# Performance work log

Hardware: AMD Instinct MI355X
Metric: run time of the kernel (lower is better)

The kernel has to match this reference:

```python
import jax, jax.numpy as jnp
import numpy as np

IN, H, F2, OUT, B = 257, 400, 600, 257, 16384


def setup_inputs() -> dict:
    key = jax.random.key(0)
    ks = jax.random.split(key, 32)
    n = lambda i, shape, s: jax.random.normal(ks[i], shape, jnp.float32) * s
    d = {
        "x": n(0, (IN, B), 1.0),
        "h1": n(1, (H, B), 1.0),
        "h2": n(2, (H, B), 1.0),
        # fc1: 257 -> 400
        "W_fc1": n(3, (H, IN), 0.05),
        "b_fc1": n(4, (H,), 0.05),
        # GRU layer 1 (hidden 400)
        "Wiz1": n(5, (H, H), 0.05), "Wir1": n(6, (H, H), 0.05), "Win1": n(7, (H, H), 0.05),
        "Whz1": n(8, (H, H), 0.05), "Whr1": n(9, (H, H), 0.05), "Whn1": n(10, (H, H), 0.05),
        "biz1": n(11, (H,), 0.05), "bir1": n(12, (H,), 0.05), "bin1": n(13, (H,), 0.05),
        "bhz1": n(14, (H,), 0.05), "bhr1": n(15, (H,), 0.05), "bhn1": n(16, (H,), 0.05),
        # GRU layer 2
        "Wiz2": n(17, (H, H), 0.05), "Wir2": n(18, (H, H), 0.05), "Win2": n(19, (H, H), 0.05),
        "Whz2": n(20, (H, H), 0.05), "Whr2": n(21, (H, H), 0.05), "Whn2": n(22, (H, H), 0.05),
        "biz2": n(23, (H,), 0.05), "bir2": n(24, (H,), 0.05), "bin2": n(25, (H,), 0.05),
        "bhz2": n(26, (H,), 0.05), "bhr2": n(27, (H,), 0.05), "bhn2": n(28, (H,), 0.05),
        # fc2: 400 -> 600, fc3: 600 -> 600, fc4: 600 -> 257
        "W_fc2": n(29, (F2, H), 0.05), "b_fc2": n(30, (F2,), 0.05),
        "W_fc3": n(31, (F2, F2), 0.05), "b_fc3": jnp.zeros((F2,), jnp.float32),
        "W_fc4": jax.random.normal(jax.random.fold_in(key, 100), (OUT, F2), jnp.float32) * 0.05,
        "b_fc4": jnp.zeros((OUT,), jnp.float32),
    }
    return d


def _gru_cell(xin, h, Wiz, Wir, Win, Whz, Whr, Whn, biz, bir, bin_, bhz, bhr, bhn):
    # xin: [H, B], h: [H, B]; column-vector convention W @ x, matching the source.
    r = jax.nn.sigmoid(Wir @ xin + bir[:, None] + Whr @ h + bhr[:, None])
    z = jax.nn.sigmoid(Wiz @ xin + biz[:, None] + Whz @ h + bhz[:, None])
    n_ = jnp.tanh(Win @ xin + bin_[:, None] + r * (Whn @ h + bhn[:, None]))
    return (1.0 - z) * n_ + z * h


def reference(x, h1, h2, W_fc1, b_fc1,
              Wiz1, Wir1, Win1, Whz1, Whr1, Whn1,
              biz1, bir1, bin1, bhz1, bhr1, bhn1,
              Wiz2, Wir2, Win2, Whz2, Whr2, Whn2,
              biz2, bir2, bin2, bhz2, bhr2, bhn2,
              W_fc2, b_fc2, W_fc3, b_fc3, W_fc4, b_fc4):
    fc1 = W_fc1 @ x + b_fc1[:, None]                       # [400, B]
    h1n = _gru_cell(fc1, h1, Wiz1, Wir1, Win1, Whz1, Whr1, Whn1,
                    biz1, bir1, bin1, bhz1, bhr1, bhn1)    # [400, B]
    h2n = _gru_cell(h1n, h2, Wiz2, Wir2, Win2, Whz2, Whr2, Whn2,
                    biz2, bir2, bin2, bhz2, bhr2, bhn2)    # [400, B]
    y = jax.nn.relu(W_fc2 @ h2n + b_fc2[:, None])          # [600, B]
    y = jax.nn.relu(W_fc3 @ y + b_fc3[:, None])            # [600, B]
    return jax.nn.sigmoid(W_fc4 @ y + b_fc4[:, None])      # [257, B]
```

## Files before the change

### kernel.cpp

```cpp
#include <hip/hip_runtime.h>
#include <math.h>


#define B_TOTAL 16384
#define H16_TOTAL 3452928L
#define PREP_TOTAL 3460352L

typedef _Float16 h8 __attribute__((ext_vector_type(8)));
typedef _Float16 h4 __attribute__((ext_vector_type(4)));
typedef float f4 __attribute__((ext_vector_type(4)));

#define GLL(g, l) __builtin_amdgcn_global_load_lds(                         \
    (const __attribute__((address_space(1))) void*)(g),                     \
    (__attribute__((address_space(3))) void*)(l), 16, 0, 0)

__device__ inline int swzg(int row, int c) { return row * 8 + (c ^ (row & 7)); }

__device__ inline void swz_bt_mt(int bid, int& bt, int& mt) {
  const int xcd = bid & 7;
  const int i = bid >> 3;
  bt = xcd * 16 + (i & 15);
  mt = i >> 4;
}

__constant__ int kJsrc[32] = {3, 5,6,7, 8,9,10, 17,18,19, 20,21,22, 29, 31, 33,
                              4, 11,12,13, 14,15,16, 23,24,25, 26,27,28, 30, 32, 34};
__constant__ int kJM[32]   = {400, 400,400,400, 400,400,400, 400,400,400, 400,400,400, 600, 600, 257,
                              400, 400,400,400, 400,400,400, 400,400,400, 400,400,400, 600, 600, 257};
__constant__ int kJK[32]   = {257, 400,400,400, 400,400,400, 400,400,400, 400,400,400, 400, 600, 600,
                              1,1,1,1, 1,1,1, 1,1,1, 1,1,1, 1, 1, 1};
__constant__ int kJKp[32]  = {320, 448,448,448, 448,448,448, 448,448,448, 448,448,448, 448, 640, 640,
                              1,1,1,1, 1,1,1, 1,1,1, 1,1,1, 1, 1, 1};
__constant__ long kJcum[33] = {0,143360,344064,544768,745472,946176,1146880,1347584,1548288,1748992,
  1949696,2150400,2351104,2551808,2838528,3248128,3452928,3453376,3453824,3454272,3454720,3455168,
  3455616,3456064,3456512,3456960,3457408,3457856,3458304,3458752,3459392,3460032,3460352};

struct SrcPtrs { const float* p[35]; };

__global__ __launch_bounds__(256) void prep_weights(SrcPtrs sp, _Float16* __restrict__ w16,
                                                    float* __restrict__ b32) {
  long w = (long)blockIdx.x * 256 + threadIdx.x;
  if (w >= PREP_TOTAL) return;
  int j = 0;
  #pragma unroll 1
  while (j < 31 && kJcum[j + 1] <= w) j++;
  long local = w - kJcum[j];
  int Kp = kJKp[j];
  int m = (int)(local / Kp);
  int k = (int)(local - (long)m * Kp);
  float v = 0.f;
  if (m < kJM[j] && k < kJK[j]) v = sp.p[kJsrc[j]][(long)m * kJK[j] + k];
  if (j < 16) w16[w] = (_Float16)v;
  else        b32[w - H16_TOTAL] = v;
}

__global__ __launch_bounds__(256) void transpose_in(const float* __restrict__ x,
                                                    const float* __restrict__ h1,
                                                    const float* __restrict__ h2,
                                                    _Float16* __restrict__ dx,
                                                    _Float16* __restrict__ dh1,
                                                    _Float16* __restrict__ dh2) {
  __shared__ float t[32][33];
  int b = blockIdx.x;
  const float* src; _Float16* dst; int F, nFT;
  if (b < 5120)        { src = x;  dst = dx;  F = 257; nFT = 10; }
  else if (b < 12288)  { b -= 5120;  src = h1; dst = dh1; F = 400; nFT = 14; }
  else                 { b -= 12288; src = h2; dst = dh2; F = 400; nFT = 14; }
  const int Fp = nFT * 32;
  const int ft = b % nFT;
  const int bt = b / nFT;
  const int ci = threadIdx.x & 31, ri = threadIdx.x >> 5;
  #pragma unroll
  for (int p = 0; p < 4; ++p) {
    int f = ft * 32 + ri + p * 8;
    float v = (f < F) ? src[(long)f * B_TOTAL + bt * 32 + ci] : 0.f;
    t[ri + p * 8][ci] = v;
  }
  __syncthreads();
  #pragma unroll
  for (int p = 0; p < 4; ++p) {
    int bb = bt * 32 + ri + p * 8;
    dst[(long)bb * Fp + ft * 32 + ci] = (_Float16)t[ci][ri + p * 8];
  }
}

__global__ __launch_bounds__(256) void transpose_out(const float* __restrict__ src,
                                                     float* __restrict__ dst) {
  __shared__ float t[32][33];
  const int nFT = 10;
  const int ft = blockIdx.x % nFT;
  const int bt = blockIdx.x / nFT;
  const int ci = threadIdx.x & 31, ri = threadIdx.x >> 5;
  #pragma unroll
  for (int p = 0; p < 4; ++p)
    t[ri + p * 8][ci] = src[(long)(bt * 32 + ri + p * 8) * 320 + ft * 32 + ci];
  __syncthreads();
  #pragma unroll
  for (int p = 0; p < 4; ++p) {
    int f = ft * 32 + ri + p * 8;
    if (f < 257) dst[(long)f * B_TOTAL + bt * 32 + ci] = t[ci][ri + p * 8];
  }
}

template <int ACT, int OUTF32>
__global__ __launch_bounds__(256) void gemm_tn(const _Float16* __restrict__ A,
                                               const _Float16* __restrict__ W,
                                               const float* __restrict__ bias,
                                               void* __restrict__ C, int K, int M) {
  __shared__ __align__(16) _Float16 As2[2][128 * 64];
  __shared__ __align__(16) _Float16 Ws2[2][64 * 64];
  const int tid = threadIdx.x;
  const int l = tid & 63;
  const int w = tid >> 6;
  int bt, mt;
  swz_bt_mt(blockIdx.x, bt, mt);
  const int wr = w >> 1, wc = w & 1;
  const int sc = ((l & 7) ^ (l >> 3)) * 8;

  const _Float16* ag = A + (long)(bt * 128 + w * 32 + (l >> 3)) * K + sc;
  const _Float16* wg = W + (long)(mt * 64 + w * 16 + (l >> 3)) * K + sc;

  f4 acc[4][2];
  #pragma unroll
  for (int i = 0; i < 4; ++i)
    #pragma unroll
    for (int jj = 0; jj < 2; ++jj) acc[i][jj] = (f4){0.f, 0.f, 0.f, 0.f};

  const int lg = l >> 4;
  const int arow = wr * 64 + (l & 15);
  const int wrow = wc * 32 + (l & 15);
  const int KT = K >> 6;

  auto stage = [&](int b, int kt) {
    const _Float16* s = ag + kt * 64;
    char* ab = (char*)(As2[b]) + w * 4096;
    #pragma unroll
    for (int i = 0; i < 4; ++i) GLL(s + (long)i * 8 * K, ab + i * 1024);
    const _Float16* s2 = wg + kt * 64;
    char* wb = (char*)(Ws2[b]) + w * 2048;
    #pragma unroll
    for (int i = 0; i < 2; ++i) GLL(s2 + (long)i * 8 * K, wb + i * 1024);
  };

  stage(0, 0);
  __syncthreads();
  int cur = 0;
  for (int t = 0; t < KT; ++t) {
    if (t + 1 < KT) stage(cur ^ 1, t + 1);
    const h8* AsV = (const h8*)(As2[cur]);
    const h8* WsV = (const h8*)(Ws2[cur]);
    h8 bfr[2][2];
    #pragma unroll
    for (int fn = 0; fn < 2; ++fn) {
      bfr[fn][0] = WsV[swzg(wrow + fn * 16, lg)];
      bfr[fn][1] = WsV[swzg(wrow + fn * 16, 4 | lg)];
    }
    #pragma unroll
    for (int fm = 0; fm < 4; ++fm) {
      h8 a0 = AsV[swzg(arow + fm * 16, lg)];
      h8 a1 = AsV[swzg(arow + fm * 16, 4 | lg)];
      #pragma unroll
      for (int fn = 0; fn < 2; ++fn) {
        acc[fm][fn] = __builtin_amdgcn_mfma_f32_16x16x32_f16(a0, bfr[fn][0], acc[fm][fn], 0, 0, 0);
        acc[fm][fn] = __builtin_amdgcn_mfma_f32_16x16x32_f16(a1, bfr[fn][1], acc[fm][fn], 0, 0, 0);
      }
    }
    __syncthreads();
    cur ^= 1;
  }

  const int colBase = mt * 64 + wc * 32 + (l & 15);
  const int rowBase = bt * 128 + wr * 64 + (l >> 4) * 4;
  #pragma unroll
  for (int fn = 0; fn < 2; ++fn) {
    const float bb = bias[colBase + fn * 16];
    #pragma unroll
    for (int fm = 0; fm < 4; ++fm) {
      #pragma unroll
      for (int r = 0; r < 4; ++r) {
        float x = acc[fm][fn][r] + bb;
        if (ACT == 1) x = fmaxf(x, 0.f);
        if (ACT == 2) x = 1.f / (1.f + __expf(-x));
        const long off = (long)(rowBase + fm * 16 + r) * M + colBase + fn * 16;
        if (OUTF32) ((float*)C)[off] = x;
        else        ((_Float16*)C)[off] = (_Float16)x;
      }
    }
  }
}

__global__ __launch_bounds__(256) void gemm_gru(const _Float16* __restrict__ Ax,
                                                const _Float16* __restrict__ Ah,
                                                const _Float16* __restrict__ Wi_,
                                                const _Float16* __restrict__ Wh_,
                                                const float* __restrict__ bi,
                                                const float* __restrict__ bh,
                                                _Float16* __restrict__ Hn) {
  __shared__ __align__(16) _Float16 As2[2][128 * 64];
  __shared__ __align__(16) _Float16 Ws2[2][3][64 * 64];
  const int tid = threadIdx.x;
  const int l = tid & 63;
  const int w = tid >> 6;
  int bt, mt;
  swz_bt_mt(blockIdx.x, bt, mt);
  const int wr = w >> 1, wc = w & 1;
  const int sc = ((l & 7) ^ (l >> 3)) * 8;

  const long arowg = (long)(bt * 128 + w * 32 + (l >> 3)) * 448 + sc;
  const long wrowg = (long)(mt * 64 + w * 16 + (l >> 3)) * 448 + sc;

  f4 acc[3][4][2];
  #pragma unroll
  for (int g = 0; g < 3; ++g)
    #pragma unroll
    for (int i = 0; i < 4; ++i)
      #pragma unroll
      for (int jj = 0; jj < 2; ++jj) acc[g][i][jj] = (f4){0.f, 0.f, 0.f, 0.f};
  h4 nxp[4][2];

  const int lg = l >> 4;
  const int arow = wr * 64 + (l & 15);
  const int wrow = wc * 32 + (l & 15);
  const int colBase = mt * 64 + wc * 32 + (l & 15);
  const float bnx0 = bi[896 + colBase], bnx1 = bi[896 + colBase + 16];

  auto stage = [&](int b, int kt) {
    const int kh = kt >= 7;
    const _Float16* As_ = kh ? Ah : Ax;
    const _Float16* Ws_ = kh ? Wh_ : Wi_;
    const int kc = (kt - (kh ? 7 : 0)) * 64;
    const _Float16* s = As_ + arowg + kc;
    char* ab = (char*)(As2[b]) + w * 4096;
    #pragma unroll
    for (int i = 0; i < 4; ++i) GLL(s + (long)i * 8 * 448, ab + i * 1024);
    const _Float16* s2 = Ws_ + wrowg + kc;
    char* wb = (char*)(Ws2[b]) + w * 2048;
    #pragma unroll
    for (int g = 0; g < 3; ++g) {
      GLL(s2 + (long)g * 200704, wb + g * 8192);
      GLL(s2 + (long)g * 200704 + 8 * 448, wb + g * 8192 + 1024);
    }
  };

  auto ktOf = [&](int i) { return i < 7 ? i : 7 + ((mt + i - 6) % 7); };

  stage(0, 0);
  __syncthreads();
  int cur = 0;
  for (int i = 0; i < 14; ++i) {
    if (i < 13) stage(cur ^ 1, ktOf(i + 1));
    const h8* AsV = (const h8*)(As2[cur]);
    const h8* WsV = (const h8*)(Ws2[cur][0]);
    h8 a[4][2];
    #pragma unroll
    for (int fm = 0; fm < 4; ++fm) {
      a[fm][0] = AsV[swzg(arow + fm * 16, lg)];
      a[fm][1] = AsV[swzg(arow + fm * 16, 4 | lg)];
    }
    #pragma unroll
    for (int g = 0; g < 3; ++g) {
      h8 b00 = WsV[g * 512 + swzg(wrow, lg)];
      h8 b01 = WsV[g * 512 + swzg(wrow, 4 | lg)];
      h8 b10 = WsV[g * 512 + swzg(wrow + 16, lg)];
      h8 b11 = WsV[g * 512 + swzg(wrow + 16, 4 | lg)];
      #pragma unroll
      for (int fm = 0; fm < 4; ++fm) {
        acc[g][fm][0] = __builtin_amdgcn_mfma_f32_16x16x32_f16(a[fm][0], b00, acc[g][fm][0], 0, 0, 0);
        acc[g][fm][0] = __builtin_amdgcn_mfma_f32_16x16x32_f16(a[fm][1], b01, acc[g][fm][0], 0, 0, 0);
        acc[g][fm][1] = __builtin_amdgcn_mfma_f32_16x16x32_f16(a[fm][0], b10, acc[g][fm][1], 0, 0, 0);
        acc[g][fm][1] = __builtin_amdgcn_mfma_f32_16x16x32_f16(a[fm][1], b11, acc[g][fm][1], 0, 0, 0);
      }
    }
    if (i == 6) {
      #pragma unroll
      for (int fm = 0; fm < 4; ++fm)
        #pragma unroll
        for (int fn = 0; fn < 2; ++fn) {
          const float bb = fn ? bnx1 : bnx0;
          #pragma unroll
          for (int r = 0; r < 4; ++r) nxp[fm][fn][r] = (_Float16)(acc[2][fm][fn][r] + bb);
          acc[2][fm][fn] = (f4){0.f, 0.f, 0.f, 0.f};
        }
    }
    __syncthreads();
    if (i < 13) cur ^= 1;
  }

  const _Float16* Alast = As2[cur];
  const int jloc = wc * 32 + (l & 15);
  const int rowLoc = wr * 64 + (l >> 4) * 4;
  const long rowGlob = (long)bt * 128 + rowLoc;
  #pragma unroll
  for (int fn = 0; fn < 2; ++fn) {
    const int j = colBase + fn * 16;
    const float bz = bi[j] + bh[j];
    const float br = bi[448 + j] + bh[448 + j];
    const float bnh = bh[896 + j];
    #pragma unroll
    for (int fm = 0; fm < 4; ++fm) {
      #pragma unroll
      for (int r = 0; r < 4; ++r) {
        const float zz = 1.f / (1.f + __expf(-(acc[0][fm][fn][r] + bz)));
        const float rr = 1.f / (1.f + __expf(-(acc[1][fm][fn][r] + br)));
        const float nn = (float)nxp[fm][fn][r] + rr * (acc[2][fm][fn][r] + bnh);
        const float th = 1.f - 2.f / (__expf(2.f * nn) + 1.f);
        const int row = rowLoc + fm * 16 + r;
        const int col = jloc + fn * 16;
        const float ho = (float)Alast[swzg(row, col >> 3) * 8 + (col & 7)];
        Hn[(rowGlob + fm * 16 + r) * 448 + j] = (_Float16)((1.f - zz) * th + zz * ho);
      }
    }
  }
}

extern "C" void kernel_launch(void* const* d_in, const int* in_sizes, int n_in,
                              void* d_out, int out_size, void* d_ws, size_t ws_size,
                              hipStream_t stream) {
  char* ws = (char*)d_ws;
  _Float16* W16  = (_Float16*)(ws);
  float*    BIAS = (float*)(ws + 6905856L);
  _Float16* buf2 = (_Float16*)(ws + 6935552L);
  _Float16* buf3 = (_Float16*)(ws + 27907072L);
  _Float16* buf4 = (_Float16*)(ws + 48878592L);
  _Float16* buf5 = (_Float16*)(ws + 63558656L);
  _Float16* buf6 = (_Float16*)(ws + 78238720L);
  float* outT = (float*)buf2;
  if (ws_size < 92918784UL) return;

  SrcPtrs sp;
  for (int i = 0; i < 35; ++i) sp.p[i] = (const float*)d_in[i];

  prep_weights<<<dim3(13517), dim3(256), 0, stream>>>(sp, W16, BIAS);
  transpose_in<<<dim3(19456), dim3(256), 0, stream>>>((const float*)d_in[0], (const float*)d_in[1],
                                                      (const float*)d_in[2], buf2, buf4, buf5);

  gemm_tn<0, 0><<<dim3(128 * 7), dim3(256), 0, stream>>>(buf2, W16, BIAS, (void*)buf3, 320, 448);
  gemm_gru<<<dim3(128 * 7), dim3(256), 0, stream>>>(buf3, buf4, W16 + 143360, W16 + 745472,
                                                    BIAS + 448, BIAS + 1792, buf6);
  gemm_gru<<<dim3(128 * 7), dim3(256), 0, stream>>>(buf6, buf5, W16 + 1347584, W16 + 1949696,
                                                    BIAS + 3136, BIAS + 4480, buf4);
  gemm_tn<1, 0><<<dim3(128 * 10), dim3(256), 0, stream>>>(buf4, W16 + 2551808, BIAS + 5824, (void*)buf2, 448, 640);
  gemm_tn<1, 0><<<dim3(128 * 10), dim3(256), 0, stream>>>(buf2, W16 + 2838528, BIAS + 6464, (void*)buf3, 640, 640);
  gemm_tn<2, 1><<<dim3(128 * 5), dim3(256), 0, stream>>>(buf3, W16 + 3248128, BIAS + 7104, (void*)outT, 640, 320);

  transpose_out<<<dim3(10 * 512), dim3(256), 0, stream>>>(outT, (float*)d_out);
}
```

Measured before the change: 408.8 us.

## Use 8-wave blocks for GEMM and GRU kernels with LDS-staged coalesced stores

Both the generic GEMM and the fused GRU GEMM move from 4 to 8 waves per block, so each wave owns a 32x32 output sub-tile and holds fewer accumulators. The GRU kernel keeps a separate fourth accumulator for the input-side n gate instead of spilling it to half precision at the midpoint. Epilogues now write fp16 results through an LDS scratch tile so global stores are 16-byte coalesced. K and M become template constants so the K loop fully unrolls. The aim is higher occupancy and better latency hiding, at the cost of an extra barrier and LDS round-trip in the epilogue.

```diff
diff --git a/kernel.cpp b/kernel.cpp
--- a/kernel.cpp
+++ b/kernel.cpp
@@ -7,12 +7,13 @@
 #define PREP_TOTAL 3460352L
 
 typedef _Float16 h8 __attribute__((ext_vector_type(8)));
-typedef _Float16 h4 __attribute__((ext_vector_type(4)));
 typedef float f4 __attribute__((ext_vector_type(4)));
 
 #define GLL(g, l) __builtin_amdgcn_global_load_lds(                         \
     (const __attribute__((address_space(1))) void*)(g),                     \
     (__attribute__((address_space(3))) void*)(l), 16, 0, 0)
+
+#define MFMA(d, a_, b_) d = __builtin_amdgcn_mfma_f32_16x16x32_f16(a_, b_, d, 0, 0, 0)
 
 __device__ inline int swzg(int row, int c) { return row * 8 + (c ^ (row & 7)); }
 
@@ -102,11 +103,12 @@
   }
 }
 
-template <int ACT, int OUTF32>
-__global__ __launch_bounds__(256) void gemm_tn(const _Float16* __restrict__ A,
-                                               const _Float16* __restrict__ W,
-                                               const float* __restrict__ bias,
-                                               void* __restrict__ C, int K, int M) {
+template <int ACT, int OUTF32, int K, int M>
+__global__ __launch_bounds__(512, 6) void gemm_tn(const _Float16* __restrict__ A,
+                                                  const _Float16* __restrict__ W,
+                                                  const float* __restrict__ bias,
+                                                  void* __restrict__ C) {
+  constexpr int KT = K / 64;
   __shared__ __align__(16) _Float16 As2[2][128 * 64];
   __shared__ __align__(16) _Float16 Ws2[2][64 * 64];
   const int tid = threadIdx.x;
@@ -116,86 +118,94 @@
   swz_bt_mt(blockIdx.x, bt, mt);
   const int wr = w >> 1, wc = w & 1;
   const int sc = ((l & 7) ^ (l >> 3)) * 8;
-
-  const _Float16* ag = A + (long)(bt * 128 + w * 32 + (l >> 3)) * K + sc;
-  const _Float16* wg = W + (long)(mt * 64 + w * 16 + (l >> 3)) * K + sc;
-
-  f4 acc[4][2];
-  #pragma unroll
-  for (int i = 0; i < 4; ++i)
+  const int srow = tid >> 3;
+
+  const _Float16* ag = A + (long)(bt * 128 + srow) * K + sc;
+  const _Float16* wg = W + (long)(mt * 64 + srow) * K + sc;
+
+  f4 acc[2][2];
+  #pragma unroll
+  for (int i = 0; i < 2; ++i)
     #pragma unroll
     for (int jj = 0; jj < 2; ++jj) acc[i][jj] = (f4){0.f, 0.f, 0.f, 0.f};
 
   const int lg = l >> 4;
-  const int arow = wr * 64 + (l & 15);
+  const int arow = wr * 32 + (l & 15);
   const int wrow = wc * 32 + (l & 15);
-  const int KT = K >> 6;
-
-  auto stage = [&](int b, int kt) {
-    const _Float16* s = ag + kt * 64;
-    char* ab = (char*)(As2[b]) + w * 4096;
-    #pragma unroll
-    for (int i = 0; i < 4; ++i) GLL(s + (long)i * 8 * K, ab + i * 1024);
-    const _Float16* s2 = wg + kt * 64;
-    char* wb = (char*)(Ws2[b]) + w * 2048;
-    #pragma unroll
-    for (int i = 0; i < 2; ++i) GLL(s2 + (long)i * 8 * K, wb + i * 1024);
+
+  auto stage = [&](int b, int t) {
+    GLL(ag + t * 64, (char*)As2[b] + w * 1024);
+    GLL(ag + t * 64 + (long)64 * K, (char*)As2[b] + w * 1024 + 8192);
+    GLL(wg + t * 64, (char*)Ws2[b] + w * 1024);
   };
 
   stage(0, 0);
   __syncthreads();
-  int cur = 0;
-  for (int t = 0; t < KT; ++t) {
-    if (t + 1 < KT) stage(cur ^ 1, t + 1);
-    const h8* AsV = (const h8*)(As2[cur]);
-    const h8* WsV = (const h8*)(Ws2[cur]);
-    h8 bfr[2][2];
-    #pragma unroll
-    for (int fn = 0; fn < 2; ++fn) {
-      bfr[fn][0] = WsV[swzg(wrow + fn * 16, lg)];
-      bfr[fn][1] = WsV[swzg(wrow + fn * 16, 4 | lg)];
-    }
-    #pragma unroll
-    for (int fm = 0; fm < 4; ++fm) {
+  #pragma unroll
+  for (int i = 0; i < KT; ++i) {
+    if (i + 1 < KT) stage((i + 1) & 1, i + 1);
+    const h8* AsV = (const h8*)As2[i & 1];
+    const h8* WsV = (const h8*)Ws2[i & 1];
+    h8 b00 = WsV[swzg(wrow, lg)],      b01 = WsV[swzg(wrow, 4 | lg)];
+    h8 b10 = WsV[swzg(wrow + 16, lg)], b11 = WsV[swzg(wrow + 16, 4 | lg)];
+    #pragma unroll
+    for (int fm = 0; fm < 2; ++fm) {
       h8 a0 = AsV[swzg(arow + fm * 16, lg)];
       h8 a1 = AsV[swzg(arow + fm * 16, 4 | lg)];
+      MFMA(acc[fm][0], a0, b00); MFMA(acc[fm][0], a1, b01);
+      MFMA(acc[fm][1], a0, b10); MFMA(acc[fm][1], a1, b11);
+    }
+    __syncthreads();
+  }
+
+  const int jloc = wc * 32 + (l & 15);
+  const int colBase = mt * 64 + jloc;
+  if (OUTF32) {
+    const int rowBase = bt * 128 + wr * 32 + (l >> 4) * 4;
+    #pragma unroll
+    for (int fn = 0; fn < 2; ++fn) {
+      const float bb = bias[colBase + fn * 16];
       #pragma unroll
-      for (int fn = 0; fn < 2; ++fn) {
-        acc[fm][fn] = __builtin_amdgcn_mfma_f32_16x16x32_f16(a0, bfr[fn][0], acc[fm][fn], 0, 0, 0);
-        acc[fm][fn] = __builtin_amdgcn_mfma_f32_16x16x32_f16(a1, bfr[fn][1], acc[fm][fn], 0, 0, 0);
-      }
+      for (int fm = 0; fm < 2; ++fm)
+        #pragma unroll
+        for (int r = 0; r < 4; ++r) {
+          float x = acc[fm][fn][r] + bb;
+          if (ACT == 2) x = 1.f / (1.f + __expf(-x));
+          ((float*)C)[(long)(rowBase + fm * 16 + r) * M + colBase + fn * 16] = x;
+        }
+    }
+  } else {
+    _Float16* scr = (_Float16*)As2;
+    const int rowLoc = wr * 32 + (l >> 4) * 4;
+    #pragma unroll
+    for (int fn = 0; fn < 2; ++fn) {
+      const float bb = bias[colBase + fn * 16];
+      #pragma unroll
+      for (int fm = 0; fm < 2; ++fm)
+        #pragma unroll
+        for (int r = 0; r < 4; ++r) {
+          float x = acc[fm][fn][r] + bb;
+          if (ACT == 1) x = fmaxf(x, 0.f);
+          scr[(rowLoc + fm * 16 + r) * 72 + jloc + fn * 16] = (_Float16)x;
+        }
     }
     __syncthreads();
-    cur ^= 1;
-  }
-
-  const int colBase = mt * 64 + wc * 32 + (l & 15);
-  const int rowBase = bt * 128 + wr * 64 + (l >> 4) * 4;
-  #pragma unroll
-  for (int fn = 0; fn < 2; ++fn) {
-    const float bb = bias[colBase + fn * 16];
-    #pragma unroll
-    for (int fm = 0; fm < 4; ++fm) {
-      #pragma unroll
-      for (int r = 0; r < 4; ++r) {
-        float x = acc[fm][fn][r] + bb;
-        if (ACT == 1) x = fmaxf(x, 0.f);
-        if (ACT == 2) x = 1.f / (1.f + __expf(-x));
-        const long off = (long)(rowBase + fm * 16 + r) * M + colBase + fn * 16;
-        if (OUTF32) ((float*)C)[off] = x;
-        else        ((_Float16*)C)[off] = (_Float16)x;
-      }
-    }
-  }
-}
-
-__global__ __launch_bounds__(256) void gemm_gru(const _Float16* __restrict__ Ax,
-                                                const _Float16* __restrict__ Ah,
-                                                const _Float16* __restrict__ Wi_,
-                                                const _Float16* __restrict__ Wh_,
-                                                const float* __restrict__ bi,
-                                                const float* __restrict__ bh,
-                                                _Float16* __restrict__ Hn) {
+    const int rrow = tid >> 2, rq = tid & 3;
+    h8 v0 = *(const h8*)(scr + rrow * 72 + rq * 16);
+    h8 v1 = *(const h8*)(scr + rrow * 72 + rq * 16 + 8);
+    _Float16* gp = (_Float16*)C + (long)(bt * 128 + rrow) * M + mt * 64 + rq * 16;
+    *(h8*)gp = v0;
+    *(h8*)(gp + 8) = v1;
+  }
+}
+
+__global__ __launch_bounds__(512, 4) void gemm_gru(const _Float16* __restrict__ Ax,
+                                                   const _Float16* __restrict__ Ah,
+                                                   const _Float16* __restrict__ Wi_,
+                                                   const _Float16* __restrict__ Wh_,
+                                                   const float* __restrict__ bi,
+                                                   const float* __restrict__ bh,
+                                                   _Float16* __restrict__ Hn) {
   __shared__ __align__(16) _Float16 As2[2][128 * 64];
   __shared__ __align__(16) _Float16 Ws2[2][3][64 * 64];
   const int tid = threadIdx.x;
@@ -205,112 +215,90 @@
   swz_bt_mt(blockIdx.x, bt, mt);
   const int wr = w >> 1, wc = w & 1;
   const int sc = ((l & 7) ^ (l >> 3)) * 8;
-
-  const long arowg = (long)(bt * 128 + w * 32 + (l >> 3)) * 448 + sc;
-  const long wrowg = (long)(mt * 64 + w * 16 + (l >> 3)) * 448 + sc;
-
-  f4 acc[3][4][2];
-  #pragma unroll
-  for (int g = 0; g < 3; ++g)
-    #pragma unroll
-    for (int i = 0; i < 4; ++i)
+  const int srow = tid >> 3;
+
+  const long arowg = (long)(bt * 128 + srow) * 448 + sc;
+  const long wrowg = (long)(mt * 64 + srow) * 448 + sc;
+
+  f4 acc[4][2][2];
+  #pragma unroll
+  for (int g = 0; g < 4; ++g)
+    #pragma unroll
+    for (int i = 0; i < 2; ++i)
       #pragma unroll
       for (int jj = 0; jj < 2; ++jj) acc[g][i][jj] = (f4){0.f, 0.f, 0.f, 0.f};
-  h4 nxp[4][2];
 
   const int lg = l >> 4;
-  const int arow = wr * 64 + (l & 15);
+  const int arow = wr * 32 + (l & 15);
   const int wrow = wc * 32 + (l & 15);
-  const int colBase = mt * 64 + wc * 32 + (l & 15);
-  const float bnx0 = bi[896 + colBase], bnx1 = bi[896 + colBase + 16];
-
-  auto stage = [&](int b, int kt) {
-    const int kh = kt >= 7;
-    const _Float16* As_ = kh ? Ah : Ax;
-    const _Float16* Ws_ = kh ? Wh_ : Wi_;
-    const int kc = (kt - (kh ? 7 : 0)) * 64;
-    const _Float16* s = As_ + arowg + kc;
-    char* ab = (char*)(As2[b]) + w * 4096;
-    #pragma unroll
-    for (int i = 0; i < 4; ++i) GLL(s + (long)i * 8 * 448, ab + i * 1024);
-    const _Float16* s2 = Ws_ + wrowg + kc;
-    char* wb = (char*)(Ws2[b]) + w * 2048;
+
+  auto stage = [&](int b, int i) {
+    const _Float16* ab = (i >= 7) ? Ah : Ax;
+    const _Float16* wb = (i >= 7) ? Wh_ : Wi_;
+    const int kc = ((i >= 7) ? (mt + i - 6) % 7 : i) * 64;
+    GLL(ab + arowg + kc, (char*)As2[b] + w * 1024);
+    GLL(ab + arowg + kc + 64 * 448, (char*)As2[b] + w * 1024 + 8192);
+    #pragma unroll
+    for (int g = 0; g < 3; ++g)
+      GLL(wb + wrowg + (long)g * 200704 + kc, (char*)Ws2[b][g] + w * 1024);
+  };
+
+  stage(0, 0);
+  __syncthreads();
+  #pragma unroll
+  for (int i = 0; i < 14; ++i) {
+    if (i < 13) stage((i + 1) & 1, i + 1);
+    const h8* AsV = (const h8*)As2[i & 1];
+    const h8* WsV = (const h8*)Ws2[i & 1][0];
+    h8 a00 = AsV[swzg(arow, lg)],      a01 = AsV[swzg(arow, 4 | lg)];
+    h8 a10 = AsV[swzg(arow + 16, lg)], a11 = AsV[swzg(arow + 16, 4 | lg)];
     #pragma unroll
     for (int g = 0; g < 3; ++g) {
-      GLL(s2 + (long)g * 200704, wb + g * 8192);
-      GLL(s2 + (long)g * 200704 + 8 * 448, wb + g * 8192 + 1024);
-    }
-  };
-
-  auto ktOf = [&](int i) { return i < 7 ? i : 7 + ((mt + i - 6) % 7); };
-
-  stage(0, 0);
-  __syncthreads();
-  int cur = 0;
-  for (int i = 0; i < 14; ++i) {
-    if (i < 13) stage(cur ^ 1, ktOf(i + 1));
-    const h8* AsV = (const h8*)(As2[cur]);
-    const h8* WsV = (const h8*)(Ws2[cur][0]);
-    h8 a[4][2];
-    #pragma unroll
-    for (int fm = 0; fm < 4; ++fm) {
-      a[fm][0] = AsV[swzg(arow + fm * 16, lg)];
-      a[fm][1] = AsV[swzg(arow + fm * 16, 4 | lg)];
-    }
-    #pragma unroll
-    for (int g = 0; g < 3; ++g) {
+      const int d = (g == 2) ? ((i < 7) ? 2 : 3) : g;
       h8 b00 = WsV[g * 512 + swzg(wrow, lg)];
       h8 b01 = WsV[g * 512 + swzg(wrow, 4 | lg)];
       h8 b10 = WsV[g * 512 + swzg(wrow + 16, lg)];
       h8 b11 = WsV[g * 512 + swzg(wrow + 16, 4 | lg)];
-      #pragma unroll
-      for (int fm = 0; fm < 4; ++fm) {
-        acc[g][fm][0] = __builtin_amdgcn_mfma_f32_16x16x32_f16(a[fm][0], b00, acc[g][fm][0], 0, 0, 0);
-        acc[g][fm][0] = __builtin_amdgcn_mfma_f32_16x16x32_f16(a[fm][1], b01, acc[g][fm][0], 0, 0, 0);
-        acc[g][fm][1] = __builtin_amdgcn_mfma_f32_16x16x32_f16(a[fm][0], b10, acc[g][fm][1], 0, 0, 0);
-        acc[g][fm][1] = __builtin_amdgcn_mfma_f32_16x16x32_f16(a[fm][1], b11, acc[g][fm][1], 0, 0, 0);
-      }
-    }
-    if (i == 6) {
-      #pragma unroll
-      for (int fm = 0; fm < 4; ++fm)
-        #pragma unroll
-        for (int fn = 0; fn < 2; ++fn) {
-          const float bb = fn ? bnx1 : bnx0;
-          #pragma unroll
-          for (int r = 0; r < 4; ++r) nxp[fm][fn][r] = (_Float16)(acc[2][fm][fn][r] + bb);
-          acc[2][fm][fn] = (f4){0.f, 0.f, 0.f, 0.f};
-        }
+      MFMA(acc[d][0][0], a00, b00); MFMA(acc[d][0][0], a01, b01);
+      MFMA(acc[d][0][1], a00, b10); MFMA(acc[d][0][1], a01, b11);
+      MFMA(acc[d][1][0], a10, b00); MFMA(acc[d][1][0], a11, b01);
+      MFMA(acc[d][1][1], a10, b10); MFMA(acc[d][1][1], a11, b11);
     }
     __syncthreads();
-    if (i < 13) cur ^= 1;
-  }
-
-  const _Float16* Alast = As2[cur];
+  }
+
+  const _Float16* Alast = As2[1];
+  _Float16* scr = (_Float16*)Ws2;
   const int jloc = wc * 32 + (l & 15);
-  const int rowLoc = wr * 64 + (l >> 4) * 4;
-  const long rowGlob = (long)bt * 128 + rowLoc;
+  const int rowLoc = wr * 32 + (l >> 4) * 4;
   #pragma unroll
   for (int fn = 0; fn < 2; ++fn) {
-    const int j = colBase + fn * 16;
+    const int j = mt * 64 + jloc + fn * 16;
     const float bz = bi[j] + bh[j];
     const float br = bi[448 + j] + bh[448 + j];
-    const float bnh = bh[896 + j];
-    #pragma unroll
-    for (int fm = 0; fm < 4; ++fm) {
+    const float bnx = bi[896 + j], bnh = bh[896 + j];
+    #pragma unroll
+    for (int fm = 0; fm < 2; ++fm) {
       #pragma unroll
       for (int r = 0; r < 4; ++r) {
         const float zz = 1.f / (1.f + __expf(-(acc[0][fm][fn][r] + bz)));
         const float rr = 1.f / (1.f + __expf(-(acc[1][fm][fn][r] + br)));
-        const float nn = (float)nxp[fm][fn][r] + rr * (acc[2][fm][fn][r] + bnh);
+        const float nn = (acc[2][fm][fn][r] + bnx) + rr * (acc[3][fm][fn][r] + bnh);
         const float th = 1.f - 2.f / (__expf(2.f * nn) + 1.f);
         const int row = rowLoc + fm * 16 + r;
         const int col = jloc + fn * 16;
         const float ho = (float)Alast[swzg(row, col >> 3) * 8 + (col & 7)];
-        Hn[(rowGlob + fm * 16 + r) * 448 + j] = (_Float16)((1.f - zz) * th + zz * ho);
+        scr[row * 72 + col] = (_Float16)((1.f - zz) * th + zz * ho);
       }
     }
   }
+  __syncthreads();
+  const int rrow = tid >> 2, rq = tid & 3;
+  h8 v0 = *(const h8*)(scr + rrow * 72 + rq * 16);
+  h8 v1 = *(const h8*)(scr + rrow * 72 + rq * 16 + 8);
+  _Float16* gp = Hn + (long)(bt * 128 + rrow) * 448 + mt * 64 + rq * 16;
+  *(h8*)gp = v0;
+  *(h8*)(gp + 8) = v1;
 }
 
 extern "C" void kernel_launch(void* const* d_in, const int* in_sizes, int n_in,
@@ -334,14 +322,14 @@
   transpose_in<<<dim3(19456), dim3(256), 0, stream>>>((const float*)d_in[0], (const float*)d_in[1],
                                                       (const float*)d_in[2], buf2, buf4, buf5);
 
-  gemm_tn<0, 0><<<dim3(128 * 7), dim3(256), 0, stream>>>(buf2, W16, BIAS, (void*)buf3, 320, 448);
-  gemm_gru<<<dim3(128 * 7), dim3(256), 0, stream>>>(buf3, buf4, W16 + 143360, W16 + 745472,
+  gemm_tn<0, 0, 320, 448><<<dim3(128 * 7), dim3(512), 0, stream>>>(buf2, W16, BIAS, (void*)buf3);
+  gemm_gru<<<dim3(128 * 7), dim3(512), 0, stream>>>(buf3, buf4, W16 + 143360, W16 + 745472,
                                                     BIAS + 448, BIAS + 1792, buf6);
-  gemm_gru<<<dim3(128 * 7), dim3(256), 0, stream>>>(buf6, buf5, W16 + 1347584, W16 + 1949696,
+  gemm_gru<<<dim3(128 * 7), dim3(512), 0, stream>>>(buf6, buf5, W16 + 1347584, W16 + 1949696,
                                                     BIAS + 3136, BIAS + 4480, buf4);
-  gemm_tn<1, 0><<<dim3(128 * 10), dim3(256), 0, stream>>>(buf4, W16 + 2551808, BIAS + 5824, (void*)buf2, 448, 640);
-  gemm_tn<1, 0><<<dim3(128 * 10), dim3(256), 0, stream>>>(buf2, W16 + 2838528, BIAS + 6464, (void*)buf3, 640, 640);
-  gemm_tn<2, 1><<<dim3(128 * 5), dim3(256), 0, stream>>>(buf3, W16 + 3248128, BIAS + 7104, (void*)outT, 640, 320);
+  gemm_tn<1, 0, 448, 640><<<dim3(128 * 10), dim3(512), 0, stream>>>(buf4, W16 + 2551808, BIAS + 5824, (void*)buf2);
+  gemm_tn<1, 0, 640, 640><<<dim3(128 * 10), dim3(512), 0, stream>>>(buf2, W16 + 2838528, BIAS + 6464, (void*)buf3);
+  gemm_tn<2, 1, 640, 320><<<dim3(128 * 5), dim3(512), 0, stream>>>(buf3, W16 + 3248128, BIAS + 7104, (void*)outT);
 
   transpose_out<<<dim3(10 * 512), dim3(256), 0, stream>>>(outT, (float*)d_out);
 }
```

Result: faster. 395.0 us (-3.4%).
